# Performance work log

Hardware: AMD Instinct MI355X
Metric: run time of the kernel (lower is better)

Reference implementation:

```python
import jax, jax.numpy as jnp
import numpy as np

EPS = 1e-5

@jax.custom_vjp
def binarize(x):
    # sign quantization: {-1, +1} (0 -> +1), as in BinaryNet Binarize
    return jnp.where(x >= 0, 1.0, -1.0).astype(x.dtype)

def _bin_fwd(x):
    return binarize(x), x

def _bin_bwd(res, g):
    # straight-through estimator with hardtanh clipping
    return (g * (jnp.abs(res) <= 1.0).astype(g.dtype),)

binarize.defvjp(_bin_fwd, _bin_bwd)


def batchnorm(x, gamma, beta):
    # BatchNorm1d, training mode: biased batch statistics over the batch axis
    mu = jnp.mean(x, axis=0)
    var = jnp.var(x, axis=0)
    return (x - mu) * jax.lax.rsqrt(var + EPS) * gamma + beta


def setup_inputs() -> dict:
    key = jax.random.key(0)
    ks = jax.random.split(key, 5)
    B, IND, HID, OUT = 16384, 768, 4096, 10
    return {
        "x": jax.random.normal(ks[0], (B, 784), jnp.float32),
        "w1": jax.random.normal(ks[1], (HID, IND), jnp.float32) * 0.05,
        "w2": jax.random.normal(ks[2], (HID, HID), jnp.float32) * 0.05,
        "w3": jax.random.normal(ks[3], (HID, HID), jnp.float32) * 0.05,
        "w4": jax.random.normal(ks[4], (OUT, HID), jnp.float32) * 0.05,
        "g1": jnp.ones(HID, jnp.float32), "b1": jnp.zeros(HID, jnp.float32),
        "g2": jnp.ones(HID, jnp.float32), "b2": jnp.zeros(HID, jnp.float32),
        "g3": jnp.ones(HID, jnp.float32), "b3": jnp.zeros(HID, jnp.float32),
        "g4": jnp.ones(OUT, jnp.float32), "b4": jnp.zeros(OUT, jnp.float32),
    }


def reference(x, w1, w2, w3, w4, g1, b1, g2, b2, g3, b3, g4, b4):
    # x.view(-1, 784); if width == 784, keep first 768 features
    h = x.reshape(-1, 784)[:, :768]
    # BinarizeLinear: binarize activations (width != 784) and weights, then matmul
    h = binarize(h) @ binarize(w1).T            # [B, 4096]
    h = jnp.clip(batchnorm(h, g1, b1), -1.0, 1.0)  # bn1 + hardtanh1
    h = binarize(h) @ binarize(w2).T
    h = jnp.clip(batchnorm(h, g2, b2), -1.0, 1.0)
    h = binarize(h) @ binarize(w3).T
    h = jnp.clip(batchnorm(h, g3, b3), -1.0, 1.0)
    h = binarize(h) @ binarize(w4).T            # [B, 10]
    h = batchnorm(h, g4, b4)
    return jax.nn.log_softmax(h, axis=1)
```

## Files before the change

### kernel.cpp

```cpp
#include <hip/hip_runtime.h>
#include <hip/hip_bf16.h>
#include <stdint.h>

typedef int v4i __attribute__((ext_vector_type(4)));

#define DEVI static __device__ __forceinline__

DEVI void gload16(const void* g, void* l) {
    __builtin_amdgcn_global_load_lds(
        (const __attribute__((address_space(1))) void*)g,
        (__attribute__((address_space(3))) void*)l,
        16, 0, 0);
}

#define WAITV(n)  asm volatile("s_waitcnt vmcnt(" #n ")" ::: "memory")
#define WAITL0()  do { asm volatile("s_waitcnt lgkmcnt(0)" ::: "memory"); \
                       __builtin_amdgcn_sched_barrier(0); } while (0)
#define SBAR()    __builtin_amdgcn_s_barrier()

__global__ __launch_bounds__(256) void k_bin_f32_to_i8(
    const float* __restrict__ w, int8_t* __restrict__ o, int n16)
{
    int t = blockIdx.x * 256 + threadIdx.x;
    if (t >= n16) return;
    const float4* s = (const float4*)w + (size_t)t * 4;
    union { int4 v; int8_t b[16]; } u;
#pragma unroll
    for (int i = 0; i < 4; ++i) {
        float4 f = s[i];
        u.b[i*4+0] = (f.x >= 0.f) ? (int8_t)1 : (int8_t)-1;
        u.b[i*4+1] = (f.y >= 0.f) ? (int8_t)1 : (int8_t)-1;
        u.b[i*4+2] = (f.z >= 0.f) ? (int8_t)1 : (int8_t)-1;
        u.b[i*4+3] = (f.w >= 0.f) ? (int8_t)1 : (int8_t)-1;
    }
    *(int4*)(o + (size_t)t * 16) = u.v;
}

__global__ __launch_bounds__(256) void k_bin_x(
    const float* __restrict__ x, int8_t* __restrict__ o)
{
    int t = blockIdx.x * 256 + threadIdx.x;
    int row = t / 48;
    int ch  = t % 48;
    const float4* s = (const float4*)(x + (size_t)row * 784 + ch * 16);
    union { int4 v; int8_t b[16]; } u;
#pragma unroll
    for (int i = 0; i < 4; ++i) {
        float4 f = s[i];
        u.b[i*4+0] = (f.x >= 0.f) ? (int8_t)1 : (int8_t)-1;
        u.b[i*4+1] = (f.y >= 0.f) ? (int8_t)1 : (int8_t)-1;
        u.b[i*4+2] = (f.z >= 0.f) ? (int8_t)1 : (int8_t)-1;
        u.b[i*4+3] = (f.w >= 0.f) ? (int8_t)1 : (int8_t)-1;
    }
    *(int4*)(o + (size_t)row * 768 + ch * 16) = u.v;
}

__global__ __launch_bounds__(512, 2)
void k_gemm256(const int8_t* __restrict__ A, const int8_t* __restrict__ B,
               int16_t* __restrict__ C, int* __restrict__ gsum,
               unsigned long long* __restrict__ gsq,
               int N, int K, int nbx)
{
    __shared__ __align__(16) int8_t lds[131072];

    const int tid  = threadIdx.x;
    const int lane = tid & 63;
    const int wave = tid >> 6;

    const int cpx = gridDim.x >> 3;
    const int id  = blockIdx.x;
    const int sw  = (id & 7) * cpx + (id >> 3);
    const int bx  = sw % nbx;
    const int by  = sw / nbx;

    const int NT = K >> 6;

    const int sr  = tid >> 2;
    const int asw = (((tid & 3) ^ ((sr >> 1) & 3)) << 4);
    const int8_t* gA0 = A + (size_t)(by * 256 + sr)       * K + asw;
    const int8_t* gA1 = A + (size_t)(by * 256 + 128 + sr) * K + asw;
    const int8_t* gB0 = B + (size_t)(bx * 256 + sr)       * K + asw;
    const int8_t* gB1 = B + (size_t)(bx * 256 + 128 + sr) * K + asw;
    const int ld0 = (wave * 64) << 4;
    const int ld1 = ld0 + 8192;

    const int lrow = lane & 15;
    const int ksl  = lane >> 4;
    const int wr = (wave >> 2) * 128;
    const int wc = (wave & 3) * 64;
    const int fsw = ((ksl ^ ((lrow >> 1) & 3)) << 4);
    int aoff[8], boff[4];
#pragma unroll
    for (int m = 0; m < 8; ++m) aoff[m] = ((wr + m * 16 + lrow) << 6) + fsw;
#pragma unroll
    for (int n = 0; n < 4; ++n) boff[n] = ((wc + n * 16 + lrow) << 6) + fsw;

    v4i acc[8][4];
    v4i zero = {0, 0, 0, 0};
#pragma unroll
    for (int m = 0; m < 8; ++m)
#pragma unroll
        for (int n = 0; n < 4; ++n) acc[m][n] = zero;

#define STAGE_A(kt) do { const int _o = (kt) << 6; const int _b = ((kt) & 3) * 16384; \
        gload16(gA0 + _o, lds + _b + ld0); gload16(gA1 + _o, lds + _b + ld1); } while (0)
#define STAGE_B(kt) do { const int _o = (kt) << 6; const int _b = ((kt) & 3) * 16384; \
        gload16(gB0 + _o, lds + 65536 + _b + ld0); gload16(gB1 + _o, lds + 65536 + _b + ld1); } while (0)

    STAGE_A(0); STAGE_B(0);
    STAGE_A(1); STAGE_B(1);
    STAGE_A(2); STAGE_B(2);
    WAITV(8);
    SBAR();

    for (int kt = 0; kt < NT; ++kt) {
        const int8_t* ab = lds + ((kt & 3) * 16384);
        const int8_t* bb = lds + 65536 + ((kt & 3) * 16384);

        v4i af[4], bf[4];
#pragma unroll
        for (int m = 0; m < 4; ++m) af[m] = *(const v4i*)(ab + aoff[m]);
#pragma unroll
        for (int n = 0; n < 4; ++n) bf[n] = *(const v4i*)(bb + boff[n]);
        if (kt + 3 < NT) STAGE_A(kt + 3);
        SBAR();
        WAITL0();
        __builtin_amdgcn_s_setprio(1);
#pragma unroll
        for (int m = 0; m < 4; ++m)
#pragma unroll
            for (int n = 0; n < 4; ++n)
                acc[m][n] = __builtin_amdgcn_mfma_i32_16x16x64_i8(
                    af[m], bf[n], acc[m][n], 0, 0, 0);
        __builtin_amdgcn_s_setprio(0);
        SBAR();

        v4i ag[4];
#pragma unroll
        for (int m = 0; m < 4; ++m) ag[m] = *(const v4i*)(ab + aoff[4 + m]);
        if (kt + 3 < NT) STAGE_B(kt + 3);
        if (kt < NT - 3)       { WAITV(8); }
        else if (kt == NT - 3) { WAITV(4); }
        else if (kt == NT - 2) { WAITV(0); }
        SBAR();
        WAITL0();
        __builtin_amdgcn_s_setprio(1);
#pragma unroll
        for (int m = 0; m < 4; ++m)
#pragma unroll
            for (int n = 0; n < 4; ++n)
                acc[4 + m][n] = __builtin_amdgcn_mfma_i32_16x16x64_i8(
                    ag[m], bf[n], acc[4 + m][n], 0, 0, 0);
        __builtin_amdgcn_s_setprio(0);
        SBAR();
    }
#undef STAGE_A
#undef STAGE_B

    const int row0 = by * 256 + wr + ksl * 4;
    const int col0 = bx * 256 + wc + lrow;
#pragma unroll
    for (int m = 0; m < 8; ++m)
#pragma unroll
        for (int rr = 0; rr < 4; ++rr) {
            int16_t* dst = C + (size_t)(row0 + m * 16 + rr) * N + col0;
#pragma unroll
            for (int n = 0; n < 4; ++n)
                dst[n * 16] = (int16_t)acc[m][n][rr];
        }
#pragma unroll
    for (int n = 0; n < 4; ++n) {
        int s = 0; unsigned q = 0;
#pragma unroll
        for (int m = 0; m < 8; ++m)
#pragma unroll
            for (int rr = 0; rr < 4; ++rr) {
                int v = acc[m][n][rr];
                s += v;
                q += (unsigned)(v * v);
            }
        s += __shfl_xor(s, 16);
        s += __shfl_xor(s, 32);
        q += (unsigned)__shfl_xor((int)q, 16);
        q += (unsigned)__shfl_xor((int)q, 32);
        if (ksl == 0) {
            const int col = col0 + n * 16;
            atomicAdd(&gsum[col], s);
            atomicAdd(&gsq[col], (unsigned long long)q);
        }
    }
}

__global__ __launch_bounds__(256)
void k_gemm4(const int8_t* __restrict__ A, const int8_t* __restrict__ Bw,
             int* __restrict__ C4, int K)
{
    const int lane = threadIdx.x & 63;
    const int wave = threadIdx.x >> 6;
    const int lrow = lane & 15, ksl = lane >> 4;
    const int r0 = blockIdx.x * 128 + wave * 32;
    const int k0 = blockIdx.y * 512;

    const int8_t* ap0 = A + (size_t)(r0 + lrow) * K + k0 + ksl * 16;
    const int8_t* ap1 = ap0 + (size_t)16 * K;
    const int8_t* bp  = Bw + (size_t)lrow * K + k0 + ksl * 16;

    v4i acc0 = {0,0,0,0}, acc1 = {0,0,0,0};
#pragma unroll
    for (int kk = 0; kk < 8; ++kk) {
        v4i a0 = *(const v4i*)(ap0 + kk * 64);
        v4i a1 = *(const v4i*)(ap1 + kk * 64);
        v4i b  = *(const v4i*)(bp  + kk * 64);
        acc0 = __builtin_amdgcn_mfma_i32_16x16x64_i8(a0, b, acc0, 0, 0, 0);
        acc1 = __builtin_amdgcn_mfma_i32_16x16x64_i8(a1, b, acc1, 0, 0, 0);
    }
#pragma unroll
    for (int rr = 0; rr < 4; ++rr) {
        atomicAdd(&C4[(size_t)(r0 + ksl * 4 + rr) * 16 + lrow], acc0[rr]);
        atomicAdd(&C4[(size_t)(r0 + 16 + ksl * 4 + rr) * 16 + lrow], acc1[rr]);
    }
}

__global__ __launch_bounds__(256)
void k_colstats4(const int* __restrict__ C4, int rows,
                 int* __restrict__ gsum, unsigned long long* __restrict__ gsq)
{
    const int col = threadIdx.x & 15, grp = threadIdx.x >> 4;
    const int rpb = rows / gridDim.x;
    const int r0  = blockIdx.x * rpb;
    int s = 0; unsigned long long q = 0;
    for (int r = grp; r < rpb; r += 16) {
        int v = C4[(size_t)(r0 + r) * 16 + col];
        s += v;
        q += (unsigned long long)((long long)v * (long long)v);
    }
    __shared__ int ss[256];
    __shared__ unsigned long long sq[256];
    ss[threadIdx.x] = s; sq[threadIdx.x] = q;
    __syncthreads();
    if (grp == 0) {
#pragma unroll
        for (int t = 1; t < 16; ++t) { s += ss[t * 16 + col]; q += sq[t * 16 + col]; }
        atomicAdd(&gsum[col], s);
        atomicAdd(&gsq[col], q);
    }
}

__global__ __launch_bounds__(128)
void k_finalize(const int* __restrict__ gsum, const unsigned long long* __restrict__ gsq,
                const float* __restrict__ gamma, const float* __restrict__ beta,
                float* __restrict__ pa, float* __restrict__ pb,
                int rows, int ncols_act, int ncols_pad)
{
    int c = blockIdx.x * 128 + threadIdx.x;
    if (c >= ncols_pad) return;
    double mu  = (double)gsum[c] / (double)rows;
    double var = (double)(long long)gsq[c] / (double)rows - mu * mu;
    float rs = rsqrtf((float)var + 1e-5f);
    float g  = (c < ncols_act) ? gamma[c] : 0.f;
    float be = (c < ncols_act) ? beta[c]  : 0.f;
    pa[c] = rs * g;
    pb[c] = be - (float)mu * rs * g;
}

__global__ __launch_bounds__(256)
void k_bnbin(const int16_t* __restrict__ C, const float* __restrict__ pa,
             const float* __restrict__ pb, int8_t* __restrict__ Aout,
             int n16, int colmask)
{
    int t = blockIdx.x * 256 + threadIdx.x;
    if (t >= n16) return;
    const size_t base = (size_t)t * 16;
    const int c0 = (int)(base & (size_t)colmask);
    union { int4 v; short s[8]; } u0, u1;
    u0.v = *(const int4*)(C + base);
    u1.v = *(const int4*)(C + base + 8);
    float4 a[4], b[4];
#pragma unroll
    for (int i = 0; i < 4; ++i) {
        a[i] = *(const float4*)(pa + c0 + i * 4);
        b[i] = *(const float4*)(pb + c0 + i * 4);
    }
    union { int4 v; int8_t b[16]; } o;
#pragma unroll
    for (int i = 0; i < 16; ++i) {
        float y = (float)((i < 8) ? u0.s[i] : u1.s[i - 8]);
        float aa = ((const float*)&a[i >> 2])[i & 3];
        float bb = ((const float*)&b[i >> 2])[i & 3];
        o.b[i] = (y * aa + bb >= 0.f) ? (int8_t)1 : (int8_t)-1;
    }
    *(int4*)(Aout + base) = o.v;
}

__global__ __launch_bounds__(256)
void k_logsoftmax(const int* __restrict__ C4, const float* __restrict__ pa,
                  const float* __restrict__ pb, float* __restrict__ out, int rows)
{
    int r = blockIdx.x * 256 + threadIdx.x;
    if (r >= rows) return;
    const int* row = C4 + (size_t)r * 16;
    float v[10];
    float m = -1e30f;
#pragma unroll
    for (int c = 0; c < 10; ++c) {
        v[c] = (float)row[c] * pa[c] + pb[c];
        m = fmaxf(m, v[c]);
    }
    float s = 0.f;
#pragma unroll
    for (int c = 0; c < 10; ++c) s += expf(v[c] - m);
    float ls = logf(s);
#pragma unroll
    for (int c = 0; c < 10; ++c) out[(size_t)r * 10 + c] = v[c] - m - ls;
}

extern "C" void kernel_launch(void* const* d_in, const int* in_sizes, int n_in,
                              void* d_out, int out_size, void* d_ws, size_t ws_size,
                              hipStream_t stream)
{
    (void)in_sizes; (void)n_in; (void)out_size; (void)ws_size;
    const float* x  = (const float*)d_in[0];
    const float* w1 = (const float*)d_in[1];
    const float* w2 = (const float*)d_in[2];
    const float* w3 = (const float*)d_in[3];
    const float* w4 = (const float*)d_in[4];
    const float* g1 = (const float*)d_in[5];
    const float* b1 = (const float*)d_in[6];
    const float* g2 = (const float*)d_in[7];
    const float* b2 = (const float*)d_in[8];
    const float* g3 = (const float*)d_in[9];
    const float* b3 = (const float*)d_in[10];
    const float* g4 = (const float*)d_in[11];
    const float* b4 = (const float*)d_in[12];
    float* out = (float*)d_out;

    const int B = 16384, HID = 4096, IND = 768;

    char* p = (char*)d_ws;
    size_t off = 0;
    auto alloc = [&](size_t sz) -> char* {
        char* r = p + off;
        off += (sz + 255) & ~(size_t)255;
        return r;
    };
    int8_t*  W1   = (int8_t*)alloc((size_t)HID * IND);
    int8_t*  W2   = (int8_t*)alloc((size_t)HID * HID);
    int8_t*  W3   = (int8_t*)alloc((size_t)HID * HID);
    int8_t*  W4p  = (int8_t*)alloc((size_t)16 * HID);
    int8_t*  Abuf = (int8_t*)alloc((size_t)B * HID);
    int16_t* C    = (int16_t*)alloc((size_t)B * HID * 2);
    int*     C4   = (int*)alloc((size_t)B * 16 * 4);
    int*     gsum = (int*)alloc((size_t)HID * 4);
    unsigned long long* gsq = (unsigned long long*)alloc((size_t)HID * 8);
    float*   pa   = (float*)alloc((size_t)HID * 4);
    float*   pb   = (float*)alloc((size_t)HID * 4);

    hipMemsetAsync(W4p, 0, (size_t)16 * HID, stream);
    k_bin_f32_to_i8<<<(HID * IND / 16 + 255) / 256, 256, 0, stream>>>(w1, W1, HID * IND / 16);
    k_bin_f32_to_i8<<<(HID * HID / 16 + 255) / 256, 256, 0, stream>>>(w2, W2, HID * HID / 16);
    k_bin_f32_to_i8<<<(HID * HID / 16 + 255) / 256, 256, 0, stream>>>(w3, W3, HID * HID / 16);
    k_bin_f32_to_i8<<<(10 * HID / 16 + 255) / 256, 256, 0, stream>>>(w4, W4p, 10 * HID / 16);
    k_bin_x<<<B * 48 / 256, 256, 0, stream>>>(x, Abuf);

    const int nbx = HID / 256, nby = B / 256;

    hipMemsetAsync(gsum, 0, HID * 12, stream);
    k_gemm256<<<nbx * nby, 512, 0, stream>>>(Abuf, W1, C, gsum, gsq, HID, IND, nbx);
    k_finalize<<<HID / 128, 128, 0, stream>>>(gsum, gsq, g1, b1, pa, pb, B, HID, HID);
    k_bnbin<<<B * HID / 16 / 256, 256, 0, stream>>>(C, pa, pb, Abuf, B * HID / 16, HID - 1);

    hipMemsetAsync(gsum, 0, HID * 12, stream);
    k_gemm256<<<nbx * nby, 512, 0, stream>>>(Abuf, W2, C, gsum, gsq, HID, HID, nbx);
    k_finalize<<<HID / 128, 128, 0, stream>>>(gsum, gsq, g2, b2, pa, pb, B, HID, HID);
    k_bnbin<<<B * HID / 16 / 256, 256, 0, stream>>>(C, pa, pb, Abuf, B * HID / 16, HID - 1);

    hipMemsetAsync(gsum, 0, HID * 12, stream);
    k_gemm256<<<nbx * nby, 512, 0, stream>>>(Abuf, W3, C, gsum, gsq, HID, HID, nbx);
    k_finalize<<<HID / 128, 128, 0, stream>>>(gsum, gsq, g3, b3, pa, pb, B, HID, HID);
    k_bnbin<<<B * HID / 16 / 256, 256, 0, stream>>>(C, pa, pb, Abuf, B * HID / 16, HID - 1);

    hipMemsetAsync(C4, 0, (size_t)B * 16 * 4, stream);
    k_gemm4<<<dim3(B / 128, 8), 256, 0, stream>>>(Abuf, W4p, C4, HID);
    hipMemsetAsync(gsum, 0, HID * 12, stream);
    k_colstats4<<<16, 256, 0, stream>>>(C4, B, gsum, gsq);
    k_finalize<<<1, 128, 0, stream>>>(gsum, gsq, g4, b4, pa, pb, B, 10, 16);
    k_logsoftmax<<<B / 256, 256, 0, stream>>>(C4, pa, pb, out, B);
}
```

Before: 805.4 us.

## Load B fragments directly to registers and ping-pong double-buffer GEMM main loop

The B operand is no longer staged through LDS; each wave loads its B fragments straight from global memory into registers one k-tile ahead. The main loop is unrolled by two with ping-pong register buffers for A and B fragments, so the next tile's A fragments are read from LDS while the current tile's MFMAs run, and each k-tile now has one barrier instead of four. LDS use halves, but B global loads are now duplicated across the waves sharing a column block and are not coalesced through LDS, and register pressure rises.

```diff
diff --git a/kernel.cpp b/kernel.cpp
--- a/kernel.cpp
+++ b/kernel.cpp
@@ -13,10 +13,8 @@
         16, 0, 0);
 }
 
-#define WAITV(n)  asm volatile("s_waitcnt vmcnt(" #n ")" ::: "memory")
-#define WAITL0()  do { asm volatile("s_waitcnt lgkmcnt(0)" ::: "memory"); \
-                       __builtin_amdgcn_sched_barrier(0); } while (0)
-#define SBAR()    __builtin_amdgcn_s_barrier()
+#define WAITV(n) asm volatile("s_waitcnt vmcnt(" #n ")" ::: "memory")
+#define SBAR()   __builtin_amdgcn_s_barrier()
 
 __global__ __launch_bounds__(256) void k_bin_f32_to_i8(
     const float* __restrict__ w, int8_t* __restrict__ o, int n16)
@@ -61,7 +59,7 @@
                unsigned long long* __restrict__ gsq,
                int N, int K, int nbx)
 {
-    __shared__ __align__(16) int8_t lds[131072];
+    __shared__ __align__(16) int8_t lds[65536];
 
     const int tid  = threadIdx.x;
     const int lane = tid & 63;
@@ -79,8 +77,6 @@
     const int asw = (((tid & 3) ^ ((sr >> 1) & 3)) << 4);
     const int8_t* gA0 = A + (size_t)(by * 256 + sr)       * K + asw;
     const int8_t* gA1 = A + (size_t)(by * 256 + 128 + sr) * K + asw;
-    const int8_t* gB0 = B + (size_t)(bx * 256 + sr)       * K + asw;
-    const int8_t* gB1 = B + (size_t)(bx * 256 + 128 + sr) * K + asw;
     const int ld0 = (wave * 64) << 4;
     const int ld1 = ld0 + 8192;
 
@@ -89,11 +85,14 @@
     const int wr = (wave >> 2) * 128;
     const int wc = (wave & 3) * 64;
     const int fsw = ((ksl ^ ((lrow >> 1) & 3)) << 4);
-    int aoff[8], boff[4];
+    int aoff[8];
 #pragma unroll
     for (int m = 0; m < 8; ++m) aoff[m] = ((wr + m * 16 + lrow) << 6) + fsw;
-#pragma unroll
-    for (int n = 0; n < 4; ++n) boff[n] = ((wc + n * 16 + lrow) << 6) + fsw;
+
+    const int8_t* gBf[4];
+#pragma unroll
+    for (int n = 0; n < 4; ++n)
+        gBf[n] = B + (size_t)(bx * 256 + wc + n * 16 + lrow) * K + ksl * 16;
 
     v4i acc[8][4];
     v4i zero = {0, 0, 0, 0};
@@ -104,58 +103,56 @@
 
 #define STAGE_A(kt) do { const int _o = (kt) << 6; const int _b = ((kt) & 3) * 16384; \
         gload16(gA0 + _o, lds + _b + ld0); gload16(gA1 + _o, lds + _b + ld1); } while (0)
-#define STAGE_B(kt) do { const int _o = (kt) << 6; const int _b = ((kt) & 3) * 16384; \
-        gload16(gB0 + _o, lds + 65536 + _b + ld0); gload16(gB1 + _o, lds + 65536 + _b + ld1); } while (0)
-
-    STAGE_A(0); STAGE_B(0);
-    STAGE_A(1); STAGE_B(1);
-    STAGE_A(2); STAGE_B(2);
-    WAITV(8);
+#define B_LOAD(kt, dst) do { const size_t _bo = (size_t)(kt) << 6;                    \
+        _Pragma("unroll") for (int n = 0; n < 4; ++n)                                 \
+            dst[n] = *(const v4i*)(gBf[n] + _bo); } while (0)
+
+#define TILE(kt, CA, CB, NA, NB) do {                                                 \
+        if ((kt) + 1 < NT) B_LOAD((kt) + 1, NB);                                      \
+        if ((kt) + 3 < NT) STAGE_A((kt) + 3);                                         \
+        if ((kt) < NT - 3)       { WAITV(8); }                                        \
+        else if ((kt) == NT - 3) { WAITV(6); }                                        \
+        else if ((kt) == NT - 2) { WAITV(4); }                                        \
+        else                     { WAITV(0); }                                        \
+        const int8_t* _ab = lds + (((kt) & 3) * 16384);                               \
+        v4i _ag[4];                                                                   \
+        _Pragma("unroll") for (int m = 0; m < 4; ++m)                                 \
+            _ag[m] = *(const v4i*)(_ab + aoff[4 + m]);                                \
+        __builtin_amdgcn_s_setprio(1);                                                \
+        _Pragma("unroll") for (int m = 0; m < 4; ++m)                                 \
+        _Pragma("unroll") for (int n = 0; n < 4; ++n)                                 \
+            acc[m][n] = __builtin_amdgcn_mfma_i32_16x16x64_i8(                        \
+                CA[m], CB[n], acc[m][n], 0, 0, 0);                                    \
+        __builtin_amdgcn_s_setprio(0);                                                \
+        if ((kt) + 1 < NT) {                                                          \
+            const int8_t* _abN = lds + ((((kt) + 1) & 3) * 16384);                    \
+            _Pragma("unroll") for (int m = 0; m < 4; ++m)                             \
+                NA[m] = *(const v4i*)(_abN + aoff[m]);                                \
+        }                                                                             \
+        __builtin_amdgcn_s_setprio(1);                                                \
+        _Pragma("unroll") for (int m = 0; m < 4; ++m)                                 \
+        _Pragma("unroll") for (int n = 0; n < 4; ++n)                                 \
+            acc[4 + m][n] = __builtin_amdgcn_mfma_i32_16x16x64_i8(                    \
+                _ag[m], CB[n], acc[4 + m][n], 0, 0, 0);                               \
+        __builtin_amdgcn_s_setprio(0);                                                \
+        SBAR(); } while (0)
+
+    v4i aX[4], bX[4], aY[4], bY[4];
+
+    B_LOAD(0, bX);
+    STAGE_A(0); STAGE_A(1); STAGE_A(2);
+    WAITV(0);
     SBAR();
-
-    for (int kt = 0; kt < NT; ++kt) {
-        const int8_t* ab = lds + ((kt & 3) * 16384);
-        const int8_t* bb = lds + 65536 + ((kt & 3) * 16384);
-
-        v4i af[4], bf[4];
-#pragma unroll
-        for (int m = 0; m < 4; ++m) af[m] = *(const v4i*)(ab + aoff[m]);
-#pragma unroll
-        for (int n = 0; n < 4; ++n) bf[n] = *(const v4i*)(bb + boff[n]);
-        if (kt + 3 < NT) STAGE_A(kt + 3);
-        SBAR();
-        WAITL0();
-        __builtin_amdgcn_s_setprio(1);
-#pragma unroll
-        for (int m = 0; m < 4; ++m)
-#pragma unroll
-            for (int n = 0; n < 4; ++n)
-                acc[m][n] = __builtin_amdgcn_mfma_i32_16x16x64_i8(
-                    af[m], bf[n], acc[m][n], 0, 0, 0);
-        __builtin_amdgcn_s_setprio(0);
-        SBAR();
-
-        v4i ag[4];
-#pragma unroll
-        for (int m = 0; m < 4; ++m) ag[m] = *(const v4i*)(ab + aoff[4 + m]);
-        if (kt + 3 < NT) STAGE_B(kt + 3);
-        if (kt < NT - 3)       { WAITV(8); }
-        else if (kt == NT - 3) { WAITV(4); }
-        else if (kt == NT - 2) { WAITV(0); }
-        SBAR();
-        WAITL0();
-        __builtin_amdgcn_s_setprio(1);
-#pragma unroll
-        for (int m = 0; m < 4; ++m)
-#pragma unroll
-            for (int n = 0; n < 4; ++n)
-                acc[4 + m][n] = __builtin_amdgcn_mfma_i32_16x16x64_i8(
-                    ag[m], bf[n], acc[4 + m][n], 0, 0, 0);
-        __builtin_amdgcn_s_setprio(0);
-        SBAR();
+#pragma unroll
+    for (int m = 0; m < 4; ++m) aX[m] = *(const v4i*)(lds + aoff[m]);
+
+    for (int kt = 0; kt < NT; kt += 2) {
+        TILE(kt,     aX, bX, aY, bY);
+        TILE(kt + 1, aY, bY, aX, bX);
     }
 #undef STAGE_A
-#undef STAGE_B
+#undef B_LOAD
+#undef TILE
 
     const int row0 = by * 256 + wr + ksl * 4;
     const int col0 = bx * 256 + wc + lrow;
```

New measurement: 1.044 ms. +29.6%, slower.
